# Performance work log

Measured on AMD Instinct MI355X. Metric: run time of the kernel, lower is better.

The kernel has to match this reference:

```python
import jax, jax.numpy as jnp
import numpy as np

MARGIN = 1.0

def setup_inputs() -> dict:
    key = jax.random.key(0)
    k1, k2 = jax.random.split(key)
    pred = jax.random.normal(k1, (8192,), dtype=jnp.float32)
    target = jax.random.randint(k2, (8192,), 0, 20, dtype=jnp.int32)
    return {"pred": pred, "target": target}

def reference(pred, target):
    p = pred.reshape(-1)
    t = target.reshape(-1)
    # ordered pairs (i, j) with t[i] < t[j]; each unordered pair with distinct
    # targets is counted exactly once, matching the original double loop.
    mask = t[:, None] < t[None, :]            # [n, n] bool
    dp = p[None, :] - p[:, None]              # pred[j] - pred[i], [n, n]
    terms = jnp.where(mask, jnp.maximum(MARGIN - dp, 0.0), 0.0)
    count = jnp.sum(mask).astype(jnp.float32)
    total = jnp.sum(terms)
    return jnp.where(count > 0, total / count, jnp.float32(0.0))
```

## Files before the change

kernel.cpp:

```cpp
#include <hip/hip_runtime.h>

#define BLOCK  256
#define IPT    8
#define ITILE  (BLOCK * IPT)
#define TJ     64
#define SUB    16
#define TSCALE 32.0f
#define NHB    16
#define NBIN   20

__global__ __launch_bounds__(BLOCK) void prl_main(
    const float* __restrict__ pred, const int* __restrict__ targ,
    int n, int gx, int npair,
    float* __restrict__ partials,
    int*   __restrict__ hist)
{
    const int tid = threadIdx.x;

    if ((int)blockIdx.x >= npair) {
        const int hb   = blockIdx.x - npair;
        const int wave = tid >> 6;
        const int lane = tid & 63;

        int c[NBIN];
        #pragma unroll
        for (int v = 0; v < NBIN; ++v) c[v] = 0;

        const int CHUNK = NHB * BLOCK * 2;
        const int iters = (n + CHUNK - 1) / CHUNK;
        for (int it = 0; it < iters; ++it) {
            const int i0 = it * CHUNK + hb * BLOCK * 2 + tid * 2;
            const int t0 = (i0     < n) ? targ[i0]     : -1;
            const int t1 = (i0 + 1 < n) ? targ[i0 + 1] : -1;
            #pragma unroll
            for (int v = 0; v < NBIN; ++v)
                c[v] += __popcll(__ballot(t0 == v)) + __popcll(__ballot(t1 == v));
        }

        __shared__ int whist[BLOCK / 64][NBIN];
        if (lane == 0) {
            #pragma unroll
            for (int v = 0; v < NBIN; ++v) whist[wave][v] = c[v];
        }
        __syncthreads();
        if (tid < NBIN) {
            int h = 0;
            #pragma unroll
            for (int w = 0; w < BLOCK / 64; ++w) h += whist[w][tid];
            hist[hb * NBIN + tid] = h;
        }
    } else {
        __shared__ float2 sj[TJ];
        __shared__ float  wsum[BLOCK / 64];
        const int bx = blockIdx.x % gx;
        const int by = blockIdx.x / gx;
        const int i0 = bx * ITILE;
        const int j0 = by * TJ;

        float pi[IPT], Ei[IPT], s[IPT];
        #pragma unroll
        for (int m = 0; m < IPT; ++m) {
            const int i = i0 + m * BLOCK + tid;
            if (i < n) {
                const float p = pred[i];
                pi[m] = p;
                Ei[m] = __fmaf_rn(-TSCALE, (float)targ[i], p);
            } else {
                pi[m] = 0.0f; Ei[m] = -1.0e9f;
            }
            s[m] = 0.0f;
        }

        if (tid < TJ) {
            const int j = j0 + tid;
            float q, F;
            if (j < n) {
                const float pj = pred[j];
                q = 1.0f - pj;
                F = __fmaf_rn(TSCALE, (float)targ[j], q - TSCALE);
            } else {
                q = 0.0f; F = -1.0e9f;
            }
            sj[tid] = make_float2(q, F);
        }
        __syncthreads();

        #pragma unroll
        for (int sub = 0; sub < TJ / SUB; ++sub) {
            float2 r[SUB];
            #pragma unroll
            for (int k = 0; k < SUB; ++k) r[k] = sj[sub * SUB + k];
            #pragma unroll
            for (int k = 0; k < SUB; ++k) {
                const float qk = r[k].x;
                const float Fk = r[k].y;
                #pragma unroll
                for (int m = 0; m < IPT; ++m) {
                    const float g = Ei[m] + Fk;
                    const float x = pi[m] + qk;
                    s[m] += fmaxf(fminf(g, x), 0.0f);
                }
            }
        }

        float st = 0.0f;
        #pragma unroll
        for (int m = 0; m < IPT; ++m) st += s[m];
        #pragma unroll
        for (int off = 32; off; off >>= 1) st += __shfl_down(st, off);

        const int wave = tid >> 6;
        if ((tid & 63) == 0) wsum[wave] = st;
        __syncthreads();
        if (tid == 0) {
            float b = 0.0f;
            #pragma unroll
            for (int w = 0; w < BLOCK / 64; ++w) b += wsum[w];
            partials[blockIdx.x] = b;
        }
    }
}

__global__ __launch_bounds__(BLOCK) void prl_final(
    const float* __restrict__ partials, int npair,
    const int* __restrict__ hist, int n, float* __restrict__ out)
{
    __shared__ double wsum[BLOCK / 64];
    __shared__ int    hv[NBIN];
    const int tid = threadIdx.x;

    double s = 0.0;
    for (int i = tid; i < npair; i += BLOCK) s += (double)partials[i];
    #pragma unroll
    for (int off = 32; off; off >>= 1) s += __shfl_down(s, off);
    if ((tid & 63) == 0) wsum[tid >> 6] = s;

    if (tid < NBIN) {
        int h = 0;
        #pragma unroll
        for (int b = 0; b < NHB; ++b) h += hist[b * NBIN + tid];
        hv[tid] = h;
    }
    __syncthreads();

    if (tid == 0) {
        double tot = 0.0;
        #pragma unroll
        for (int w = 0; w < BLOCK / 64; ++w) tot += wsum[w];
        long long sq = 0;
        #pragma unroll
        for (int v = 0; v < NBIN; ++v) { const long long h = hv[v]; sq += h * h; }
        const long long cnt = ((long long)n * (long long)n - sq) / 2;
        out[0] = (cnt > 0) ? (float)(tot / (double)cnt) : 0.0f;
    }
}

extern "C" void kernel_launch(void* const* d_in, const int* in_sizes, int n_in,
                              void* d_out, int out_size, void* d_ws, size_t ws_size,
                              hipStream_t stream) {
    const float* pred = (const float*)d_in[0];
    const int*   targ = (const int*)d_in[1];
    float*       out  = (float*)d_out;
    const int    n    = in_sizes[0];

    float* partials = (float*)d_ws;
    int*   hist     = (int*)((char*)d_ws + ((size_t)((n + ITILE - 1) / ITILE) *
                                            ((n + TJ - 1) / TJ) + 64) * sizeof(float));

    const int gx    = (n + ITILE - 1) / ITILE;
    const int gy    = (n + TJ - 1) / TJ;
    const int npair = gx * gy;

    prl_main<<<npair + NHB, BLOCK, 0, stream>>>(pred, targ, n, gx, npair, partials, hist);
    prl_final<<<1, BLOCK, 0, stream>>>(partials, npair, hist, n, out);
}
```

Measured before the change: 15.66 us.

## Halve j-tile, move target histogram into final kernel, use float4 LDS reads

Halves the j tile from 64 to 32, which doubles the pair-block count (4x128 to 4x256 blocks) so more of the GPU is filled with less work per block. The target histogram moves out of the main kernel's extra blocks into the single-block final kernel. That removes the branch and the workspace histogram, but the final kernel must now scan all 8192 targets serially. Shared-memory j values are read as float4, two j entries per load, to cut LDS instructions.

Measured after the change: 27.90 us. 78.2% more time.

```diff
diff --git a/kernel.cpp b/kernel.cpp
--- a/kernel.cpp
+++ b/kernel.cpp
@@ -3,144 +3,122 @@
 #define BLOCK  256
 #define IPT    8
 #define ITILE  (BLOCK * IPT)
-#define TJ     64
-#define SUB    16
+#define TJ     32
+#define SUB    8
 #define TSCALE 32.0f
-#define NHB    16
 #define NBIN   20
 
-__global__ __launch_bounds__(BLOCK) void prl_main(
+__global__ __launch_bounds__(BLOCK) void prl_pairs(
     const float* __restrict__ pred, const int* __restrict__ targ,
-    int n, int gx, int npair,
-    float* __restrict__ partials,
-    int*   __restrict__ hist)
+    int n, int gx, float* __restrict__ partials)
 {
+    __shared__ float4 sj[TJ / 2];
+    __shared__ float  wsum[BLOCK / 64];
+
     const int tid = threadIdx.x;
+    const int bx  = blockIdx.x % gx;
+    const int by  = blockIdx.x / gx;
+    const int i0  = bx * ITILE;
+    const int j0  = by * TJ;
 
-    if ((int)blockIdx.x >= npair) {
-        const int hb   = blockIdx.x - npair;
-        const int wave = tid >> 6;
-        const int lane = tid & 63;
+    float pi[IPT], Ei[IPT], s[IPT];
+    #pragma unroll
+    for (int m = 0; m < IPT; ++m) {
+        const int i = i0 + m * BLOCK + tid;
+        if (i < n) {
+            const float p = pred[i];
+            pi[m] = p;
+            Ei[m] = __fmaf_rn(-TSCALE, (float)targ[i], p);
+        } else {
+            pi[m] = 0.0f; Ei[m] = -1.0e9f;
+        }
+        s[m] = 0.0f;
+    }
 
-        int c[NBIN];
+    if (tid < TJ) {
+        const int j = j0 + tid;
+        float q, F;
+        if (j < n) {
+            const float pj = pred[j];
+            q = 1.0f - pj;
+            F = __fmaf_rn(TSCALE, (float)targ[j], q - TSCALE);
+        } else {
+            q = 0.0f; F = -1.0e9f;
+        }
+        ((float2*)sj)[tid] = make_float2(q, F);
+    }
+    __syncthreads();
+
+    #pragma unroll
+    for (int sub = 0; sub < TJ / (2 * SUB); ++sub) {
+        float4 r[SUB];
         #pragma unroll
-        for (int v = 0; v < NBIN; ++v) c[v] = 0;
-
-        const int CHUNK = NHB * BLOCK * 2;
-        const int iters = (n + CHUNK - 1) / CHUNK;
-        for (int it = 0; it < iters; ++it) {
-            const int i0 = it * CHUNK + hb * BLOCK * 2 + tid * 2;
-            const int t0 = (i0     < n) ? targ[i0]     : -1;
-            const int t1 = (i0 + 1 < n) ? targ[i0 + 1] : -1;
+        for (int k = 0; k < SUB; ++k) r[k] = sj[sub * SUB + k];
+        #pragma unroll
+        for (int k = 0; k < SUB; ++k) {
             #pragma unroll
-            for (int v = 0; v < NBIN; ++v)
-                c[v] += __popcll(__ballot(t0 == v)) + __popcll(__ballot(t1 == v));
-        }
-
-        __shared__ int whist[BLOCK / 64][NBIN];
-        if (lane == 0) {
+            for (int m = 0; m < IPT; ++m) {
+                const float g = Ei[m] + r[k].y;
+                const float x = pi[m] + r[k].x;
+                s[m] += fmaxf(fminf(g, x), 0.0f);
+            }
             #pragma unroll
-            for (int v = 0; v < NBIN; ++v) whist[wave][v] = c[v];
-        }
-        __syncthreads();
-        if (tid < NBIN) {
-            int h = 0;
-            #pragma unroll
-            for (int w = 0; w < BLOCK / 64; ++w) h += whist[w][tid];
-            hist[hb * NBIN + tid] = h;
-        }
-    } else {
-        __shared__ float2 sj[TJ];
-        __shared__ float  wsum[BLOCK / 64];
-        const int bx = blockIdx.x % gx;
-        const int by = blockIdx.x / gx;
-        const int i0 = bx * ITILE;
-        const int j0 = by * TJ;
-
-        float pi[IPT], Ei[IPT], s[IPT];
-        #pragma unroll
-        for (int m = 0; m < IPT; ++m) {
-            const int i = i0 + m * BLOCK + tid;
-            if (i < n) {
-                const float p = pred[i];
-                pi[m] = p;
-                Ei[m] = __fmaf_rn(-TSCALE, (float)targ[i], p);
-            } else {
-                pi[m] = 0.0f; Ei[m] = -1.0e9f;
-            }
-            s[m] = 0.0f;
-        }
-
-        if (tid < TJ) {
-            const int j = j0 + tid;
-            float q, F;
-            if (j < n) {
-                const float pj = pred[j];
-                q = 1.0f - pj;
-                F = __fmaf_rn(TSCALE, (float)targ[j], q - TSCALE);
-            } else {
-                q = 0.0f; F = -1.0e9f;
-            }
-            sj[tid] = make_float2(q, F);
-        }
-        __syncthreads();
-
-        #pragma unroll
-        for (int sub = 0; sub < TJ / SUB; ++sub) {
-            float2 r[SUB];
-            #pragma unroll
-            for (int k = 0; k < SUB; ++k) r[k] = sj[sub * SUB + k];
-            #pragma unroll
-            for (int k = 0; k < SUB; ++k) {
-                const float qk = r[k].x;
-                const float Fk = r[k].y;
-                #pragma unroll
-                for (int m = 0; m < IPT; ++m) {
-                    const float g = Ei[m] + Fk;
-                    const float x = pi[m] + qk;
-                    s[m] += fmaxf(fminf(g, x), 0.0f);
-                }
+            for (int m = 0; m < IPT; ++m) {
+                const float g = Ei[m] + r[k].w;
+                const float x = pi[m] + r[k].z;
+                s[m] += fmaxf(fminf(g, x), 0.0f);
             }
         }
+    }
 
-        float st = 0.0f;
+    float st = 0.0f;
+    #pragma unroll
+    for (int m = 0; m < IPT; ++m) st += s[m];
+    #pragma unroll
+    for (int off = 32; off; off >>= 1) st += __shfl_down(st, off);
+
+    const int wave = tid >> 6;
+    if ((tid & 63) == 0) wsum[wave] = st;
+    __syncthreads();
+    if (tid == 0) {
+        float b = 0.0f;
         #pragma unroll
-        for (int m = 0; m < IPT; ++m) st += s[m];
-        #pragma unroll
-        for (int off = 32; off; off >>= 1) st += __shfl_down(st, off);
-
-        const int wave = tid >> 6;
-        if ((tid & 63) == 0) wsum[wave] = st;
-        __syncthreads();
-        if (tid == 0) {
-            float b = 0.0f;
-            #pragma unroll
-            for (int w = 0; w < BLOCK / 64; ++w) b += wsum[w];
-            partials[blockIdx.x] = b;
-        }
+        for (int w = 0; w < BLOCK / 64; ++w) b += wsum[w];
+        partials[blockIdx.x] = b;
     }
 }
 
 __global__ __launch_bounds__(BLOCK) void prl_final(
     const float* __restrict__ partials, int npair,
-    const int* __restrict__ hist, int n, float* __restrict__ out)
+    const int* __restrict__ targ, int n, float* __restrict__ out)
 {
     __shared__ double wsum[BLOCK / 64];
-    __shared__ int    hv[NBIN];
-    const int tid = threadIdx.x;
+    __shared__ int    whist[BLOCK / 64][NBIN];
+    const int tid  = threadIdx.x;
+    const int wave = tid >> 6;
+    const int lane = tid & 63;
+
+    int c[NBIN];
+    #pragma unroll
+    for (int v = 0; v < NBIN; ++v) c[v] = 0;
+    const int iters = (n + BLOCK - 1) / BLOCK;
+    for (int it = 0; it < iters; ++it) {
+        const int i = it * BLOCK + tid;
+        const int t = (i < n) ? targ[i] : -1;
+        #pragma unroll
+        for (int v = 0; v < NBIN; ++v)
+            c[v] += __popcll(__ballot(t == v));
+    }
+    if (lane == 0) {
+        #pragma unroll
+        for (int v = 0; v < NBIN; ++v) whist[wave][v] = c[v];
+    }
 
     double s = 0.0;
     for (int i = tid; i < npair; i += BLOCK) s += (double)partials[i];
     #pragma unroll
     for (int off = 32; off; off >>= 1) s += __shfl_down(s, off);
-    if ((tid & 63) == 0) wsum[tid >> 6] = s;
-
-    if (tid < NBIN) {
-        int h = 0;
-        #pragma unroll
-        for (int b = 0; b < NHB; ++b) h += hist[b * NBIN + tid];
-        hv[tid] = h;
-    }
+    if (lane == 0) wsum[wave] = s;
     __syncthreads();
 
     if (tid == 0) {
@@ -149,7 +127,12 @@
         for (int w = 0; w < BLOCK / 64; ++w) tot += wsum[w];
         long long sq = 0;
         #pragma unroll
-        for (int v = 0; v < NBIN; ++v) { const long long h = hv[v]; sq += h * h; }
+        for (int v = 0; v < NBIN; ++v) {
+            long long h = 0;
+            #pragma unroll
+            for (int w = 0; w < BLOCK / 64; ++w) h += whist[w][v];
+            sq += h * h;
+        }
         const long long cnt = ((long long)n * (long long)n - sq) / 2;
         out[0] = (cnt > 0) ? (float)(tot / (double)cnt) : 0.0f;
     }
@@ -164,13 +147,10 @@
     const int    n    = in_sizes[0];
 
     float* partials = (float*)d_ws;
-    int*   hist     = (int*)((char*)d_ws + ((size_t)((n + ITILE - 1) / ITILE) *
-                                            ((n + TJ - 1) / TJ) + 64) * sizeof(float));
-
     const int gx    = (n + ITILE - 1) / ITILE;
     const int gy    = (n + TJ - 1) / TJ;
     const int npair = gx * gy;
 
-    prl_main<<<npair + NHB, BLOCK, 0, stream>>>(pred, targ, n, gx, npair, partials, hist);
-    prl_final<<<1, BLOCK, 0, stream>>>(partials, npair, hist, n, out);
+    prl_pairs<<<npair, BLOCK, 0, stream>>>(pred, targ, n, gx, partials);
+    prl_final<<<1, BLOCK, 0, stream>>>(partials, npair, targ, n, out);
 }
```
